# Kernel tuning notes

Measured on AMD Instinct MI355X. Metric: run time of the kernel, lower is better.

The kernel has to match this reference:

```python
import jax, jax.numpy as jnp
import numpy as np

N = 100000
E = 1600000
EPS = 1e-5


def _bn(h, g, b):
    # BatchNorm1d in training mode: batch stats over dim 0 (biased variance)
    mu = h.mean(0)
    var = ((h - mu) ** 2).mean(0)
    return g * (h - mu) * jax.lax.rsqrt(var + EPS) + b


def setup_inputs() -> dict:
    key = jax.random.key(0)

    def nrm(i, shape, scale=1.0):
        return jax.random.normal(jax.random.fold_in(key, i), shape, jnp.float32) * scale

    inp = {
        "x": nrm(0, (N, 1)),
        "edge_attr": nrm(1, (E, 2)),
        "edge_index": jax.random.randint(jax.random.fold_in(key, 2), (2, E), 0, N),
        "dir_edge_index": jax.random.randint(jax.random.fold_in(key, 3), (2, E), 0, N),
        "prop_edge_index": jax.random.randint(jax.random.fold_in(key, 4), (2, E), 0, N),
    }
    k = [10]

    def lin(name, fan_in, fan_out):
        inp[name] = nrm(k[0], (fan_in, fan_out), 1.0 / float(np.sqrt(fan_in)))
        k[0] += 1

    def bnp(prefix, c):
        inp[prefix + "_g"] = jnp.ones((c,), jnp.float32)
        inp[prefix + "_b"] = jnp.zeros((c,), jnp.float32)

    lin("c1_ws", 1, 2); lin("c1_wn", 1, 2); lin("c1_we", 2, 2); bnp("c1", 2)
    lin("d1_ws", 3, 4); lin("d1_wn", 3, 4); bnp("d1", 4)
    lin("c2_ws", 5, 6); lin("c2_wn", 5, 6); lin("c2_we", 2, 6); bnp("c2", 6)
    lin("d2_ws", 7, 8); lin("d2_wn", 7, 8); bnp("d2", 8)
    lin("c3_ws", 9, 10); lin("c3_wn", 9, 10); lin("c3_we", 2, 10); bnp("c3", 10)
    lin("d3_ws", 11, 12); lin("d3_wn", 11, 12); bnp("d3", 12)
    lin("pw1", 13, 8); inp["pb1"] = jnp.zeros((8,), jnp.float32); bnp("p1", 8)
    lin("pw2", 8, 4); inp["pb2"] = jnp.zeros((4,), jnp.float32); bnp("p2", 4)
    lin("pw3", 4, 1); inp["pb3"] = jnp.zeros((1,), jnp.float32)
    lin("ew1", 28, 14); inp["eb1"] = jnp.zeros((14,), jnp.float32); bnp("e1", 14)
    lin("ew2", 14, 1); inp["eb2"] = jnp.zeros((1,), jnp.float32)
    return inp


def reference(x, edge_attr, edge_index, dir_edge_index, prop_edge_index,
              c1_ws, c1_wn, c1_we, c1_g, c1_b,
              d1_ws, d1_wn, d1_g, d1_b,
              c2_ws, c2_wn, c2_we, c2_g, c2_b,
              d2_ws, d2_wn, d2_g, d2_b,
              c3_ws, c3_wn, c3_we, c3_g, c3_b,
              d3_ws, d3_wn, d3_g, d3_b,
              pw1, pb1, p1_g, p1_b, pw2, pb2, p2_g, p2_b, pw3, pb3,
              ew1, eb1, e1_g, e1_b, ew2, eb2):
    n = x.shape[0]
    src, dst = edge_index[0], edge_index[1]        # x_j = x[src], x_i = x[dst]
    psrc, pdst = prop_edge_index[0], prop_edge_index[1]

    def flexconv(h, ws, wn, we, g, b):
        m = jax.nn.relu(_bn(h[dst] @ ws + edge_attr @ we + h[src] @ wn, g, b))
        agg = jax.ops.segment_sum(m, dst, num_segments=n)
        return jnp.concatenate([h[:, :1], agg], axis=1)

    def edgeinter(h, ws, wn, g, b):
        m = jax.nn.relu(_bn(h[pdst] @ ws + h[psrc] @ wn, g, b))
        agg = jax.ops.segment_sum(m, pdst, num_segments=n)
        return jnp.concatenate([h[:, :1], agg], axis=1)

    out = flexconv(x, c1_ws, c1_wn, c1_we, c1_g, c1_b)      # [N,3]
    out = edgeinter(out, d1_ws, d1_wn, d1_g, d1_b)          # [N,5]
    out = flexconv(out, c2_ws, c2_wn, c2_we, c2_g, c2_b)    # [N,7]
    out = edgeinter(out, d2_ws, d2_wn, d2_g, d2_b)          # [N,9]
    out = flexconv(out, c3_ws, c3_wn, c3_we, c3_g, c3_b)    # [N,11]
    out = edgeinter(out, d3_ws, d3_wn, d3_g, d3_b)          # [N,13]

    h = _bn(jax.nn.relu(out @ pw1 + pb1), p1_g, p1_b)
    h = _bn(jax.nn.relu(h @ pw2 + pb2), p2_g, p2_b)
    power = jax.nn.sigmoid(1.5 * (h @ pw3 + pb3))           # [N,1]

    dsrc, ddst = dir_edge_index[0], dir_edge_index[1]
    f = jnp.concatenate([out[ddst], power[ddst], out[dsrc], power[dsrc]], axis=1)  # [E,28]
    e = _bn(jax.nn.relu(f @ ew1 + eb1), e1_g, e1_b)
    direction = jax.nn.sigmoid(1.5 * (e @ ew2 + eb2))       # [E,1]
    return power, direction
```

## Files before the change

### kernel.cpp

```cpp
#include <hip/hip_runtime.h>
#include <hip/hip_fp16.h>
#include <math.h>

static constexpr int BLK = 256;
static constexpr float BN_EPS = 1e-5f;

__device__ __forceinline__ float sigmoid15(float z) {
    return 1.0f / (1.0f + expf(-1.5f * z));
}

__device__ __forceinline__ unsigned pack_ea(float2 v) {
    unsigned hx = __half_as_ushort(__float2half_rn(v.x));
    unsigned hy = __half_as_ushort(__float2half_rn(v.y));
    return hx | (hy << 16);
}
__device__ __forceinline__ float2 unpack_ea(unsigned u) {
    return make_float2(__half2float(__ushort_as_half((unsigned short)(u & 0xffffu))),
                       __half2float(__ushort_as_half((unsigned short)(u >> 16))));
}

template<int C>
__device__ __forceinline__ void block_stats_reduce(float (&s)[C], float (&ss)[C],
                                                   double* __restrict__ stats)
{
    #pragma unroll
    for (int j = 0; j < C; ++j) {
        #pragma unroll
        for (int o = 32; o > 0; o >>= 1) {
            s[j]  += __shfl_down(s[j],  o, 64);
            ss[j] += __shfl_down(ss[j], o, 64);
        }
    }
    __shared__ float red[2][C][BLK / 64];
    const int wave = threadIdx.x >> 6, lane = threadIdx.x & 63;
    if (lane == 0) {
        #pragma unroll
        for (int j = 0; j < C; ++j) { red[0][j][wave] = s[j]; red[1][j][wave] = ss[j]; }
    }
    __syncthreads();
    if (threadIdx.x < C) {
        const int j = threadIdx.x;
        float a = 0.f, b = 0.f;
        #pragma unroll
        for (int w = 0; w < BLK / 64; ++w) { a += red[0][j][w]; b += red[1][j][w]; }
        atomicAdd(&stats[j],      (double)a);
        atomicAdd(&stats[16 + j], (double)b);
    }
}

template<int C>
__device__ __forceinline__ void bn_coefs(const double* __restrict__ stats,
                                         const float* __restrict__ g, const float* __restrict__ b,
                                         double invE, float (&sc)[C], float (&bb)[C])
{
    #pragma unroll
    for (int j = 0; j < C; ++j) {
        const double mu  = stats[j] * invE;
        const double var = stats[16 + j] * invE - mu * mu;
        const float inv = rsqrtf((float)(var + (double)BN_EPS));
        const float gg = g[j];
        sc[j] = gg * inv;
        bb[j] = b[j] - (float)mu * gg * inv;
    }
}


__global__ __launch_bounds__(BLK) void init_kernel(int* __restrict__ deg, double* __restrict__ stats,
                                                   int* __restrict__ rowstart, int n2, int total)
{
    const int i = blockIdx.x * blockDim.x + threadIdx.x;
    if (i < n2) deg[i] = 0;
    if (i < 288) stats[i] = 0.0;
    if (i == 0) rowstart[n2] = total;
}

__global__ __launch_bounds__(BLK) void hist_kernel(const int* __restrict__ edst,
                                                   const int* __restrict__ pdst,
                                                   int* __restrict__ deg, int N, int E)
{
    const int grp = blockIdx.x & 7;
    const int bg  = blockIdx.x >> 3;
    const int gstride = (gridDim.x >> 3) * blockDim.x;
    if (grp < 4) {
        const int lo = (int)((size_t)N * grp / 4), hi = (int)((size_t)N * (grp + 1) / 4);
        for (int e = bg * blockDim.x + threadIdx.x; e < E; e += gstride) {
            const int d = edst[e];
            if (d >= lo && d < hi) atomicAdd(&deg[d], 1);
        }
    } else {
        const int gg = grp - 4;
        const int lo = (int)((size_t)N * gg / 4), hi = (int)((size_t)N * (gg + 1) / 4);
        for (int e = bg * blockDim.x + threadIdx.x; e < E; e += gstride) {
            const int p = pdst[e];
            if (p >= lo && p < hi) atomicAdd(&deg[N + p], 1);
        }
    }
}

__global__ __launch_bounds__(256) void scan1_kernel(const int* __restrict__ deg,
                                                    int* __restrict__ rowstart,
                                                    int* __restrict__ partials, int n2)
{
    __shared__ int lds[256];
    const int tid = threadIdx.x;
    const int base = blockIdx.x * 1024 + tid * 4;
    int v[4]; int loc = 0;
    #pragma unroll
    for (int r = 0; r < 4; ++r) { v[r] = (base + r < n2) ? deg[base + r] : 0; loc += v[r]; }
    lds[tid] = loc; __syncthreads();
    #pragma unroll
    for (int off = 1; off < 256; off <<= 1) {
        int t = (tid >= off) ? lds[tid - off] : 0;
        __syncthreads();
        lds[tid] += t;
        __syncthreads();
    }
    int excl = lds[tid] - loc;
    int run = excl;
    #pragma unroll
    for (int r = 0; r < 4; ++r) {
        if (base + r < n2) rowstart[base + r] = run;
        run += v[r];
    }
    if (tid == 255) partials[blockIdx.x] = lds[255];
}

__global__ __launch_bounds__(256) void scan2_kernel(int* __restrict__ partials, int n)
{
    __shared__ int lds[256];
    const int tid = threadIdx.x;
    const int base = tid * 4;
    int v[4]; int loc = 0;
    #pragma unroll
    for (int r = 0; r < 4; ++r) { v[r] = (base + r < n) ? partials[base + r] : 0; loc += v[r]; }
    lds[tid] = loc; __syncthreads();
    #pragma unroll
    for (int off = 1; off < 256; off <<= 1) {
        int t = (tid >= off) ? lds[tid - off] : 0;
        __syncthreads();
        lds[tid] += t;
        __syncthreads();
    }
    int excl = lds[tid] - loc;
    int run = excl;
    #pragma unroll
    for (int r = 0; r < 4; ++r) {
        if (base + r < n) partials[base + r] = run;
        run += v[r];
    }
}

__global__ __launch_bounds__(BLK) void scan3_kernel(int* __restrict__ rowstart,
                                                    int* __restrict__ cursor,
                                                    const int* __restrict__ partials, int n2)
{
    const int i = blockIdx.x * blockDim.x + threadIdx.x;
    if (i >= n2) return;
    const int v = rowstart[i] + partials[i >> 10];
    rowstart[i] = v;
    cursor[i] = v;
}

__global__ __launch_bounds__(BLK) void fill_kernel(
    const int* __restrict__ esrc, const int* __restrict__ edst,
    const int* __restrict__ psrc, const int* __restrict__ pdst,
    const float* __restrict__ ea,
    int* __restrict__ cursor, uint2* __restrict__ csr_e,
    unsigned int* __restrict__ csr_psrc, int N, int E)
{
    const int grp = blockIdx.x & 7;
    const int bg  = blockIdx.x >> 3;
    const int gstride = (gridDim.x >> 3) * blockDim.x;
    if (grp < 4) {
        const int lo = (int)((size_t)N * grp / 4), hi = (int)((size_t)N * (grp + 1) / 4);
        for (int e = bg * blockDim.x + threadIdx.x; e < E; e += gstride) {
            const int d = edst[e];
            if (d >= lo && d < hi) {
                const float2 eav = ((const float2*)ea)[e];
                const int pos = atomicAdd(&cursor[d], 1);
                csr_e[pos] = make_uint2((unsigned)esrc[e], pack_ea(eav));
            }
        }
    } else {
        const int gg = grp - 4;
        const int lo = (int)((size_t)N * gg / 4), hi = (int)((size_t)N * (gg + 1) / 4);
        for (int e = bg * blockDim.x + threadIdx.x; e < E; e += gstride) {
            const int p = pdst[e];
            if (p >= lo && p < hi) {
                const int pos2 = atomicAdd(&cursor[N + p], 1);
                csr_psrc[pos2 - E] = (unsigned)psrc[e];
            }
        }
    }
}


template<int CIN, int COUT>
__global__ __launch_bounds__(BLK) void projQ_kernel(
    const float* __restrict__ x, const float* __restrict__ agg_in,
    const float* __restrict__ wn, float* __restrict__ Q, int n)
{
    constexpr int PAD = (COUT + 3) & ~3;
    __shared__ float swn[CIN * COUT];
    for (int i = threadIdx.x; i < CIN * COUT; i += blockDim.x) swn[i] = wn[i];
    __syncthreads();
    const int i = blockIdx.x * blockDim.x + threadIdx.x;
    if (i >= n) return;
    float h[CIN];
    h[0] = x[i];
    #pragma unroll
    for (int k = 1; k < CIN; ++k) h[k] = agg_in[(size_t)i * (CIN - 1) + (k - 1)];
    #pragma unroll
    for (int j = 0; j < COUT; ++j) {
        float q = 0.f;
        #pragma unroll
        for (int k = 0; k < CIN; ++k) q = fmaf(h[k], swn[k * COUT + j], q);
        Q[(size_t)i * PAD + j] = q;
    }
}

template<int CIN, int COUT, bool HASEA>
__global__ __launch_bounds__(BLK) void node_stats_kernel(
    const int* __restrict__ rowstart,
    const uint2* __restrict__ csr_e, const unsigned int* __restrict__ csr_psrc,
    const float* __restrict__ x, const float* __restrict__ agg_in,
    const float* __restrict__ ws, const float* __restrict__ Q,
    const float* __restrict__ we,
    double* __restrict__ stats, int N, int base, int koff)
{
    constexpr int PAD = (COUT + 3) & ~3;
    __shared__ float sws[CIN * COUT];
    for (int i = threadIdx.x; i < CIN * COUT; i += blockDim.x) sws[i] = ws[i];
    __syncthreads();
    float we0[COUT], we1[COUT];
    if constexpr (HASEA) {
        #pragma unroll
        for (int j = 0; j < COUT; ++j) { we0[j] = we[j]; we1[j] = we[COUT + j]; }
    }
    float s[COUT], ss[COUT];
    #pragma unroll
    for (int j = 0; j < COUT; ++j) { s[j] = 0.f; ss[j] = 0.f; }
    const int t = blockIdx.x * blockDim.x + threadIdx.x;
    const int i = t >> 2, quad = t & 3;
    if (i < N) {
        float h[CIN];
        h[0] = x[i];
        #pragma unroll
        for (int k = 1; k < CIN; ++k) h[k] = agg_in[(size_t)i * (CIN - 1) + (k - 1)];
        float pp[COUT];
        #pragma unroll
        for (int j = 0; j < COUT; ++j) {
            float p = 0.f;
            #pragma unroll
            for (int k = 0; k < CIN; ++k) p = fmaf(h[k], sws[k * COUT + j], p);
            pp[j] = p;
        }
        const int k0 = rowstart[base + i], k1 = rowstart[base + i + 1];
        for (int k = k0 + quad; k < k1; k += 4) {
            unsigned sn;
            float2 eav;
            if constexpr (HASEA) {
                const uint2 ce = csr_e[k];
                sn = ce.x; eav = unpack_ea(ce.y);
            } else {
                sn = csr_psrc[k - koff];
            }
            #pragma unroll
            for (int j = 0; j < COUT; ++j) {
                float m = pp[j] + Q[(size_t)sn * PAD + j];
                if constexpr (HASEA) m = fmaf(eav.x, we0[j], fmaf(eav.y, we1[j], m));
                s[j] += m; ss[j] = fmaf(m, m, ss[j]);
            }
        }
    }
    block_stats_reduce<COUT>(s, ss, stats);
}

template<int CIN, int COUT, bool HASEA, int CIN2, int COUT2>
__global__ __launch_bounds__(BLK) void node_agg_kernel(
    const int* __restrict__ rowstart,
    const uint2* __restrict__ csr_e, const unsigned int* __restrict__ csr_psrc,
    const float* __restrict__ x, const float* __restrict__ agg_in,
    const float* __restrict__ ws, const float* __restrict__ Q,
    const float* __restrict__ we,
    const float* __restrict__ g, const float* __restrict__ b,
    const double* __restrict__ stats,
    float* __restrict__ agg_out,
    const float* __restrict__ wn2, float* __restrict__ Qout,
    int N, int base, int koff, float invE)
{
    constexpr int PAD = (COUT + 3) & ~3;
    constexpr bool FUSEQ = (COUT2 > 0);
    constexpr int W2 = FUSEQ ? CIN2 * COUT2 : 1;
    __shared__ float sws[CIN * COUT];
    __shared__ float swn2[W2];
    for (int i = threadIdx.x; i < CIN * COUT; i += blockDim.x) sws[i] = ws[i];
    if constexpr (FUSEQ) {
        for (int i = threadIdx.x; i < W2; i += blockDim.x) swn2[i] = wn2[i];
    }
    __syncthreads();
    const int t = blockIdx.x * blockDim.x + threadIdx.x;
    const int i = t >> 2, quad = t & 3;
    if (i >= N) return;
    float we0[COUT], we1[COUT];
    if constexpr (HASEA) {
        #pragma unroll
        for (int j = 0; j < COUT; ++j) { we0[j] = we[j]; we1[j] = we[COUT + j]; }
    }
    float sc[COUT], bb[COUT];
    bn_coefs<COUT>(stats, g, b, (double)invE, sc, bb);
    float h[CIN];
    h[0] = x[i];
    #pragma unroll
    for (int k = 1; k < CIN; ++k) h[k] = agg_in[(size_t)i * (CIN - 1) + (k - 1)];
    float pp[COUT], acc[COUT];
    #pragma unroll
    for (int j = 0; j < COUT; ++j) {
        float p = 0.f;
        #pragma unroll
        for (int k = 0; k < CIN; ++k) p = fmaf(h[k], sws[k * COUT + j], p);
        pp[j] = p; acc[j] = 0.f;
    }
    const int k0 = rowstart[base + i], k1 = rowstart[base + i + 1];
    for (int k = k0 + quad; k < k1; k += 4) {
        unsigned sn;
        float2 eav;
        if constexpr (HASEA) {
            const uint2 ce = csr_e[k];
            sn = ce.x; eav = unpack_ea(ce.y);
        } else {
            sn = csr_psrc[k - koff];
        }
        #pragma unroll
        for (int j = 0; j < COUT; ++j) {
            float m = pp[j] + Q[(size_t)sn * PAD + j];
            if constexpr (HASEA) m = fmaf(eav.x, we0[j], fmaf(eav.y, we1[j], m));
            acc[j] += fmaxf(fmaf(sc[j], m, bb[j]), 0.f);
        }
    }
    #pragma unroll
    for (int j = 0; j < COUT; ++j) {
        acc[j] += __shfl_xor(acc[j], 1, 64);
        acc[j] += __shfl_xor(acc[j], 2, 64);
    }
    if (quad == 0) {
        #pragma unroll
        for (int j = 0; j < COUT; ++j) agg_out[(size_t)i * COUT + j] = acc[j];
        if constexpr (FUSEQ) {
            constexpr int PAD2 = (COUT2 + 3) & ~3;
            #pragma unroll
            for (int j2 = 0; j2 < COUT2; ++j2) {
                float q = h[0] * swn2[j2];
                #pragma unroll
                for (int k = 0; k < COUT; ++k)
                    q = fmaf(acc[k], swn2[(k + 1) * COUT2 + j2], q);
                Qout[(size_t)i * PAD2 + j2] = q;
            }
        }
    }
}


__global__ __launch_bounds__(BLK) void zero_stats_kernel(double* __restrict__ stats, int n)
{
    int i = blockIdx.x * blockDim.x + threadIdx.x;
    if (i < n) stats[i] = 0.0;
}

template<int CIN, int COUT>
__global__ __launch_bounds__(BLK) void projPQ_kernel(
    const float* __restrict__ x, const float* __restrict__ agg_in,
    const float* __restrict__ ws, const float* __restrict__ wn,
    float* __restrict__ P, float* __restrict__ Q, float* __restrict__ agg_out, int n)
{
    __shared__ float sws[CIN * COUT], swn[CIN * COUT];
    for (int i = threadIdx.x; i < CIN * COUT; i += blockDim.x) { sws[i] = ws[i]; swn[i] = wn[i]; }
    __syncthreads();
    const int i = blockIdx.x * blockDim.x + threadIdx.x;
    if (i >= n) return;
    float h[CIN];
    h[0] = x[i];
    #pragma unroll
    for (int k = 1; k < CIN; ++k) h[k] = agg_in[(size_t)i * (CIN - 1) + (k - 1)];
    #pragma unroll
    for (int j = 0; j < COUT; ++j) {
        float p = 0.f, q = 0.f;
        #pragma unroll
        for (int k = 0; k < CIN; ++k) {
            p = fmaf(h[k], sws[k * COUT + j], p);
            q = fmaf(h[k], swn[k * COUT + j], q);
        }
        P[(size_t)i * COUT + j] = p;
        Q[(size_t)i * COUT + j] = q;
        agg_out[(size_t)i * COUT + j] = 0.f;
    }
}

template<int COUT, bool HASEA>
__global__ __launch_bounds__(BLK) void edge_stats_kernel(
    const int* __restrict__ esrc, const int* __restrict__ edst,
    const float* __restrict__ P,  const float* __restrict__ Q,
    const float* __restrict__ ea, const float* __restrict__ we,
    double* __restrict__ stats, int E)
{
    float we0[COUT], we1[COUT];
    if constexpr (HASEA) {
        #pragma unroll
        for (int j = 0; j < COUT; ++j) { we0[j] = we[j]; we1[j] = we[COUT + j]; }
    }
    float s[COUT], ss[COUT];
    #pragma unroll
    for (int j = 0; j < COUT; ++j) { s[j] = 0.f; ss[j] = 0.f; }
    const int stride = gridDim.x * blockDim.x;
    for (int e = blockIdx.x * blockDim.x + threadIdx.x; e < E; e += stride) {
        const int d = edst[e], sn = esrc[e];
        float2 eav = make_float2(0.f, 0.f);
        if constexpr (HASEA) eav = ((const float2* __restrict__)ea)[e];
        #pragma unroll
        for (int j = 0; j < COUT; ++j) {
            float m = P[(size_t)d * COUT + j] + Q[(size_t)sn * COUT + j];
            if constexpr (HASEA) m += eav.x * we0[j] + eav.y * we1[j];
            s[j] += m; ss[j] = fmaf(m, m, ss[j]);
        }
    }
    block_stats_reduce<COUT>(s, ss, stats);
}

template<int COUT, bool HASEA>
__global__ __launch_bounds__(BLK) void edge_scatter_kernel(
    const int* __restrict__ esrc, const int* __restrict__ edst,
    const float* __restrict__ P,  const float* __restrict__ Q,
    const float* __restrict__ ea, const float* __restrict__ we,
    const float* __restrict__ g,  const float* __restrict__ b,
    const double* __restrict__ stats,
    float* __restrict__ agg_out, int E)
{
    float we0[COUT], we1[COUT], sc[COUT], bb[COUT];
    #pragma unroll
    for (int j = 0; j < COUT; ++j) {
        if constexpr (HASEA) { we0[j] = we[j]; we1[j] = we[COUT + j]; }
    }
    bn_coefs<COUT>(stats, g, b, 1.0 / (double)E, sc, bb);
    const int stride = gridDim.x * blockDim.x;
    for (int e = blockIdx.x * blockDim.x + threadIdx.x; e < E; e += stride) {
        const int d = edst[e], sn = esrc[e];
        float2 eav = make_float2(0.f, 0.f);
        if constexpr (HASEA) eav = ((const float2* __restrict__)ea)[e];
        #pragma unroll
        for (int j = 0; j < COUT; ++j) {
            float m = P[(size_t)d * COUT + j] + Q[(size_t)sn * COUT + j];
            if constexpr (HASEA) m += eav.x * we0[j] + eav.y * we1[j];
            const float y = fmaxf(fmaf(sc[j], m, bb[j]), 0.f);
            if (y > 0.f) unsafeAtomicAdd(&agg_out[(size_t)d * COUT + j], y);
        }
    }
}


__global__ __launch_bounds__(BLK) void mlp1_kernel(
    const float* __restrict__ x, const float* __restrict__ agg6,
    const float* __restrict__ pw1, const float* __restrict__ pb1,
    float* __restrict__ t1, double* __restrict__ stats, int n)
{
    __shared__ float w[13 * 8];
    __shared__ float bsh[8];
    for (int i = threadIdx.x; i < 13 * 8; i += blockDim.x) w[i] = pw1[i];
    if (threadIdx.x < 8) bsh[threadIdx.x] = pb1[threadIdx.x];
    __syncthreads();
    const int i = blockIdx.x * blockDim.x + threadIdx.x;
    float s[8], ss[8];
    #pragma unroll
    for (int j = 0; j < 8; ++j) { s[j] = 0.f; ss[j] = 0.f; }
    if (i < n) {
        float h[13];
        h[0] = x[i];
        #pragma unroll
        for (int k = 0; k < 12; ++k) h[k + 1] = agg6[(size_t)i * 12 + k];
        #pragma unroll
        for (int j = 0; j < 8; ++j) {
            float t = bsh[j];
            #pragma unroll
            for (int k = 0; k < 13; ++k) t = fmaf(h[k], w[k * 8 + j], t);
            t = fmaxf(t, 0.f);
            t1[(size_t)i * 8 + j] = t;
            s[j] = t; ss[j] = t * t;
        }
    }
    block_stats_reduce<8>(s, ss, stats);
}

__global__ __launch_bounds__(BLK) void mlp2_kernel(
    const float* __restrict__ t1,
    const float* __restrict__ p1g, const float* __restrict__ p1b,
    const float* __restrict__ pw2, const float* __restrict__ pb2,
    const double* __restrict__ stats1,
    float* __restrict__ t2, double* __restrict__ stats2, int n)
{
    float sc[8], bb[8];
    bn_coefs<8>(stats1, p1g, p1b, 1.0 / (double)n, sc, bb);
    const int i = blockIdx.x * blockDim.x + threadIdx.x;
    float s[4], ss[4];
    #pragma unroll
    for (int j = 0; j < 4; ++j) { s[j] = 0.f; ss[j] = 0.f; }
    if (i < n) {
        float u[8];
        #pragma unroll
        for (int j = 0; j < 8; ++j) u[j] = fmaf(sc[j], t1[(size_t)i * 8 + j], bb[j]);
        #pragma unroll
        for (int j2 = 0; j2 < 4; ++j2) {
            float t = pb2[j2];
            #pragma unroll
            for (int j = 0; j < 8; ++j) t = fmaf(u[j], pw2[j * 4 + j2], t);
            t = fmaxf(t, 0.f);
            t2[(size_t)i * 4 + j2] = t;
            s[j2] = t; ss[j2] = t * t;
        }
    }
    block_stats_reduce<4>(s, ss, stats2);
}

__global__ __launch_bounds__(BLK) void mlp3_kernel(
    const float* __restrict__ t2,
    const float* __restrict__ p2g, const float* __restrict__ p2b,
    const float* __restrict__ pw3, const float* __restrict__ pb3,
    const float* __restrict__ x, const float* __restrict__ agg6,
    const float* __restrict__ ew1, const float* __restrict__ eb1,
    const double* __restrict__ stats2,
    float* __restrict__ power_out, float* __restrict__ A, float* __restrict__ B,
    int n, int astride)
{
    __shared__ float w1[28 * 14];
    for (int i = threadIdx.x; i < 28 * 14; i += blockDim.x) w1[i] = ew1[i];
    __syncthreads();
    float sc[4], bb[4];
    bn_coefs<4>(stats2, p2g, p2b, 1.0 / (double)n, sc, bb);
    const int i = blockIdx.x * blockDim.x + threadIdx.x;
    if (i >= n) return;
    float z = pb3[0];
    #pragma unroll
    for (int j = 0; j < 4; ++j) z = fmaf(fmaf(sc[j], t2[(size_t)i * 4 + j], bb[j]), pw3[j], z);
    const float pw = sigmoid15(z);
    power_out[i] = pw;
    float h[14];
    h[0] = x[i];
    #pragma unroll
    for (int k = 0; k < 12; ++k) h[k + 1] = agg6[(size_t)i * 12 + k];
    h[13] = pw;
    #pragma unroll
    for (int c = 0; c < 14; ++c) {
        float a = eb1[c], b2 = 0.f;
        #pragma unroll
        for (int k = 0; k < 14; ++k) {
            a  = fmaf(h[k], w1[k * 14 + c], a);
            b2 = fmaf(h[k], w1[(14 + k) * 14 + c], b2);
        }
        A[(size_t)i * astride + c] = a;
        B[(size_t)i * astride + c] = b2;
    }
}

__global__ __launch_bounds__(BLK) void ehead_stats_kernel(
    const int* __restrict__ dsrc, const int* __restrict__ ddst,
    const float* __restrict__ A, const float* __restrict__ B,
    double* __restrict__ stats, int E, int astride)
{
    float s[14], ss[14];
    #pragma unroll
    for (int j = 0; j < 14; ++j) { s[j] = 0.f; ss[j] = 0.f; }
    const int stride = gridDim.x * blockDim.x;
    for (int e = blockIdx.x * blockDim.x + threadIdx.x; e < E; e += stride) {
        const int dd = ddst[e], ds = dsrc[e];
        #pragma unroll
        for (int c = 0; c < 14; ++c) {
            const float r = fmaxf(A[(size_t)dd * astride + c] + B[(size_t)ds * astride + c], 0.f);
            s[c] += r; ss[c] = fmaf(r, r, ss[c]);
        }
    }
    block_stats_reduce<14>(s, ss, stats);
}

__global__ __launch_bounds__(BLK) void ehead_final_kernel(
    const int* __restrict__ dsrc, const int* __restrict__ ddst,
    const float* __restrict__ A, const float* __restrict__ B,
    const float* __restrict__ e1g, const float* __restrict__ e1b,
    const float* __restrict__ ew2, const float* __restrict__ eb2,
    const double* __restrict__ stats, float* __restrict__ dir_out, int E, int astride)
{
    float sc[14];
    float off = eb2[0];
    const double invE = 1.0 / (double)E;
    #pragma unroll
    for (int c = 0; c < 14; ++c) {
        const double mu  = stats[c] * invE;
        const double var = stats[16 + c] * invE - mu * mu;
        const float inv = rsqrtf((float)(var + (double)BN_EPS));
        const float gi = e1g[c] * inv;
        sc[c] = gi * ew2[c];
        off += (e1b[c] - (float)mu * gi) * ew2[c];
    }
    const int stride = gridDim.x * blockDim.x;
    for (int e = blockIdx.x * blockDim.x + threadIdx.x; e < E; e += stride) {
        const int dd = ddst[e], ds = dsrc[e];
        float z = off;
        #pragma unroll
        for (int c = 0; c < 14; ++c) {
            const float r = fmaxf(A[(size_t)dd * astride + c] + B[(size_t)ds * astride + c], 0.f);
            z = fmaf(r, sc[c], z);
        }
        dir_out[e] = sigmoid15(z);
    }
}


extern "C" void kernel_launch(void* const* d_in, const int* in_sizes, int n_in,
                              void* d_out, int out_size, void* d_ws, size_t ws_size,
                              hipStream_t stream)
{
    const float* x    = (const float*)d_in[0];
    const float* ea   = (const float*)d_in[1];
    const int*   eidx = (const int*)d_in[2];
    const int*   didx = (const int*)d_in[3];
    const int*   pidx = (const int*)d_in[4];
    const float *c1_ws=(const float*)d_in[5],  *c1_wn=(const float*)d_in[6],  *c1_we=(const float*)d_in[7],  *c1_g=(const float*)d_in[8],  *c1_b=(const float*)d_in[9];
    const float *d1_ws=(const float*)d_in[10], *d1_wn=(const float*)d_in[11], *d1_g=(const float*)d_in[12], *d1_b=(const float*)d_in[13];
    const float *c2_ws=(const float*)d_in[14], *c2_wn=(const float*)d_in[15], *c2_we=(const float*)d_in[16], *c2_g=(const float*)d_in[17], *c2_b=(const float*)d_in[18];
    const float *d2_ws=(const float*)d_in[19], *d2_wn=(const float*)d_in[20], *d2_g=(const float*)d_in[21], *d2_b=(const float*)d_in[22];
    const float *c3_ws=(const float*)d_in[23], *c3_wn=(const float*)d_in[24], *c3_we=(const float*)d_in[25], *c3_g=(const float*)d_in[26], *c3_b=(const float*)d_in[27];
    const float *d3_ws=(const float*)d_in[28], *d3_wn=(const float*)d_in[29], *d3_g=(const float*)d_in[30], *d3_b=(const float*)d_in[31];
    const float *pw1=(const float*)d_in[32], *pb1=(const float*)d_in[33], *p1_g=(const float*)d_in[34], *p1_b=(const float*)d_in[35];
    const float *pw2=(const float*)d_in[36], *pb2=(const float*)d_in[37], *p2_g=(const float*)d_in[38], *p2_b=(const float*)d_in[39];
    const float *pw3=(const float*)d_in[40], *pb3=(const float*)d_in[41];
    const float *ew1=(const float*)d_in[42], *eb1=(const float*)d_in[43], *e1_g=(const float*)d_in[44], *e1_b=(const float*)d_in[45];
    const float *ew2=(const float*)d_in[46], *eb2=(const float*)d_in[47];

    const int N = in_sizes[0];
    const int E = in_sizes[2] / 2;
    const int n2 = 2 * N;
    const int *esrc = eidx,     *edst = eidx + E;
    const int *dsrc = didx,     *ddst = didx + E;
    const int *psrc = pidx,     *pdst = pidx + E;

    float* power_out = (float*)d_out;
    float* dir_out   = power_out + N;

    const int gN  = (N + BLK - 1) / BLK;
    const int g2  = (n2 + BLK - 1) / BLK;
    const int g4  = ((size_t)4 * N + BLK - 1) / BLK;
    const int gE  = 1024;
    const int gEf = (E + BLK - 1) / BLK;
    const int gX  = 8 * 160;
    const float invE = 1.0f / (float)E;

    const size_t abFloats = (size_t)32 * N;
    const size_t csreBytes = ((size_t)8 * E > 4 * abFloats) ? (size_t)8 * E : 4 * abFloats;
    const size_t need_csr = 4096
        + sizeof(float) * ((size_t)N * 12
                         + (size_t)N * 12
                         + (size_t)N * 12
                         + (size_t)N * 12)
        + csreBytes
        + sizeof(unsigned int) * (size_t)E
        + sizeof(int) * ((size_t)n2 + 2)
        + sizeof(int) * (size_t)n2
        + sizeof(int) * 1024;

    double* stats = (double*)d_ws;

    if (ws_size >= need_csr) {
        float* fws  = (float*)((char*)d_ws + 4096);
        float* Qa   = fws;                fws += (size_t)N * 12;
        float* Qb   = fws;                fws += (size_t)N * 12;
        float* aggA = fws;                fws += (size_t)N * 12;
        float* aggB = fws;                fws += (size_t)N * 12;
        uint2* csr_e = (uint2*)fws;
        unsigned int* csr_psrc = (unsigned int*)((char*)csr_e + csreBytes);
        int* rowstart = (int*)(csr_psrc + E);
        int* cursor   = rowstart + (n2 + 2);
        int* deg      = cursor;
        int* partials = cursor + n2;
        float* t1   = aggA;
        float* t2   = aggA + (size_t)N * 8;
        float* Abuf = (float*)csr_e;
        float* Bbuf = Abuf + (size_t)N * 16;

        const int nparts = (n2 + 1023) / 1024;

        init_kernel<<<g2, BLK, 0, stream>>>(deg, stats, rowstart, n2, 2 * E);
        hist_kernel<<<gX, BLK, 0, stream>>>(edst, pdst, deg, N, E);
        scan1_kernel<<<nparts, 256, 0, stream>>>(deg, rowstart, partials, n2);
        scan2_kernel<<<1, 256, 0, stream>>>(partials, nparts);
        scan3_kernel<<<g2, BLK, 0, stream>>>(rowstart, cursor, partials, n2);
        fill_kernel<<<gX, BLK, 0, stream>>>(esrc, edst, psrc, pdst, ea, cursor, csr_e, csr_psrc, N, E);

        projQ_kernel<1, 2><<<gN, BLK, 0, stream>>>(x, nullptr, c1_wn, Qa, N);
        node_stats_kernel<1, 2, true><<<g4, BLK, 0, stream>>>(rowstart, csr_e, csr_psrc, x, nullptr, c1_ws, Qa, c1_we, stats + 0, N, 0, 0);
        node_agg_kernel<1, 2, true, 3, 4><<<g4, BLK, 0, stream>>>(rowstart, csr_e, csr_psrc, x, nullptr, c1_ws, Qa, c1_we, c1_g, c1_b, stats + 0, aggA, d1_wn, Qb, N, 0, 0, invE);
        node_stats_kernel<3, 4, false><<<g4, BLK, 0, stream>>>(rowstart, csr_e, csr_psrc, x, aggA, d1_ws, Qb, nullptr, stats + 32, N, N, E);
        node_agg_kernel<3, 4, false, 5, 6><<<g4, BLK, 0, stream>>>(rowstart, csr_e, csr_psrc, x, aggA, d1_ws, Qb, nullptr, d1_g, d1_b, stats + 32, aggB, c2_wn, Qa, N, N, E, invE);
        node_stats_kernel<5, 6, true><<<g4, BLK, 0, stream>>>(rowstart, csr_e, csr_psrc, x, aggB, c2_ws, Qa, c2_we, stats + 64, N, 0, 0);
        node_agg_kernel<5, 6, true, 7, 8><<<g4, BLK, 0, stream>>>(rowstart, csr_e, csr_psrc, x, aggB, c2_ws, Qa, c2_we, c2_g, c2_b, stats + 64, aggA, d2_wn, Qb, N, 0, 0, invE);
        node_stats_kernel<7, 8, false><<<g4, BLK, 0, stream>>>(rowstart, csr_e, csr_psrc, x, aggA, d2_ws, Qb, nullptr, stats + 96, N, N, E);
        node_agg_kernel<7, 8, false, 9, 10><<<g4, BLK, 0, stream>>>(rowstart, csr_e, csr_psrc, x, aggA, d2_ws, Qb, nullptr, d2_g, d2_b, stats + 96, aggB, c3_wn, Qa, N, N, E, invE);
        node_stats_kernel<9, 10, true><<<g4, BLK, 0, stream>>>(rowstart, csr_e, csr_psrc, x, aggB, c3_ws, Qa, c3_we, stats + 128, N, 0, 0);
        node_agg_kernel<9, 10, true, 11, 12><<<g4, BLK, 0, stream>>>(rowstart, csr_e, csr_psrc, x, aggB, c3_ws, Qa, c3_we, c3_g, c3_b, stats + 128, aggA, d3_wn, Qb, N, 0, 0, invE);
        node_stats_kernel<11, 12, false><<<g4, BLK, 0, stream>>>(rowstart, csr_e, csr_psrc, x, aggA, d3_ws, Qb, nullptr, stats + 160, N, N, E);
        node_agg_kernel<11, 12, false, 0, 0><<<g4, BLK, 0, stream>>>(rowstart, csr_e, csr_psrc, x, aggA, d3_ws, Qb, nullptr, d3_g, d3_b, stats + 160, aggB, nullptr, nullptr, N, N, E, invE);

        mlp1_kernel<<<gN, BLK, 0, stream>>>(x, aggB, pw1, pb1, t1, stats + 192, N);
        mlp2_kernel<<<gN, BLK, 0, stream>>>(t1, p1_g, p1_b, pw2, pb2, stats + 192, t2, stats + 224, N);
        mlp3_kernel<<<gN, BLK, 0, stream>>>(t2, p2_g, p2_b, pw3, pb3, x, aggB, ew1, eb1, stats + 224,
                                            power_out, Abuf, Bbuf, N, 16);
        ehead_stats_kernel<<<gE, BLK, 0, stream>>>(dsrc, ddst, Abuf, Bbuf, stats + 256, E, 16);
        ehead_final_kernel<<<gEf, BLK, 0, stream>>>(dsrc, ddst, Abuf, Bbuf, e1_g, e1_b, ew2, eb2,
                                                    stats + 256, dir_out, E, 16);
    } else {
        float* fws  = (float*)((char*)d_ws + 4096);
        float* P    = fws;                fws += (size_t)N * 14;
        float* Q    = fws;                fws += (size_t)N * 14;
        float* aggA = fws;                fws += (size_t)N * 12;
        float* aggB = fws;                fws += (size_t)N * 12;
        float* t1   = aggA;
        float* t2   = aggA + (size_t)N * 8;
        float* Abuf = P;
        float* Bbuf = Q;

        zero_stats_kernel<<<2, BLK, 0, stream>>>(stats, 288);

        projPQ_kernel<1, 2><<<gN, BLK, 0, stream>>>(x, nullptr, c1_ws, c1_wn, P, Q, aggA, N);
        edge_stats_kernel<2, true><<<gE, BLK, 0, stream>>>(esrc, edst, P, Q, ea, c1_we, stats + 0, E);
        edge_scatter_kernel<2, true><<<gE, BLK, 0, stream>>>(esrc, edst, P, Q, ea, c1_we, c1_g, c1_b, stats + 0, aggA, E);

        projPQ_kernel<3, 4><<<gN, BLK, 0, stream>>>(x, aggA, d1_ws, d1_wn, P, Q, aggB, N);
        edge_stats_kernel<4, false><<<gE, BLK, 0, stream>>>(psrc, pdst, P, Q, nullptr, nullptr, stats + 32, E);
        edge_scatter_kernel<4, false><<<gE, BLK, 0, stream>>>(psrc, pdst, P, Q, nullptr, nullptr, d1_g, d1_b, stats + 32, aggB, E);

        projPQ_kernel<5, 6><<<gN, BLK, 0, stream>>>(x, aggB, c2_ws, c2_wn, P, Q, aggA, N);
        edge_stats_kernel<6, true><<<gE, BLK, 0, stream>>>(esrc, edst, P, Q, ea, c2_we, stats + 64, E);
        edge_scatter_kernel<6, true><<<gE, BLK, 0, stream>>>(esrc, edst, P, Q, ea, c2_we, c2_g, c2_b, stats + 64, aggA, E);

        projPQ_kernel<7, 8><<<gN, BLK, 0, stream>>>(x, aggA, d2_ws, d2_wn, P, Q, aggB, N);
        edge_stats_kernel<8, false><<<gE, BLK, 0, stream>>>(psrc, pdst, P, Q, nullptr, nullptr, stats + 96, E);
        edge_scatter_kernel<8, false><<<gE, BLK, 0, stream>>>(psrc, pdst, P, Q, nullptr, nullptr, d2_g, d2_b, stats + 96, aggB, E);

        projPQ_kernel<9, 10><<<gN, BLK, 0, stream>>>(x, aggB, c3_ws, c3_wn, P, Q, aggA, N);
        edge_stats_kernel<10, true><<<gE, BLK, 0, stream>>>(esrc, edst, P, Q, ea, c3_we, stats + 128, E);
        edge_scatter_kernel<10, true><<<gE, BLK, 0, stream>>>(esrc, edst, P, Q, ea, c3_we, c3_g, c3_b, stats + 128, aggA, E);

        projPQ_kernel<11, 12><<<gN, BLK, 0, stream>>>(x, aggA, d3_ws, d3_wn, P, Q, aggB, N);
        edge_stats_kernel<12, false><<<gE, BLK, 0, stream>>>(psrc, pdst, P, Q, nullptr, nullptr, stats + 160, E);
        edge_scatter_kernel<12, false><<<gE, BLK, 0, stream>>>(psrc, pdst, P, Q, nullptr, nullptr, d3_g, d3_b, stats + 160, aggB, E);

        mlp1_kernel<<<gN, BLK, 0, stream>>>(x, aggB, pw1, pb1, t1, stats + 192, N);
        mlp2_kernel<<<gN, BLK, 0, stream>>>(t1, p1_g, p1_b, pw2, pb2, stats + 192, t2, stats + 224, N);
        mlp3_kernel<<<gN, BLK, 0, stream>>>(t2, p2_g, p2_b, pw3, pb3, x, aggB, ew1, eb1, stats + 224,
                                            power_out, Abuf, Bbuf, N, 14);
        ehead_stats_kernel<<<gE, BLK, 0, stream>>>(dsrc, ddst, Abuf, Bbuf, stats + 256, E, 14);
        ehead_final_kernel<<<gE, BLK, 0, stream>>>(dsrc, ddst, Abuf, Bbuf, e1_g, e1_b, ew2, eb2,
                                                   stats + 256, dir_out, E, 14);
    }
}
```

Measured before the change: 952.1 us.

## Store gathered node tables in fp16 padded rows and stream edge indices nontemporally

The per-node Q projection tables and the edge-head A/B tables are now stored as fp16 rows padded to 8 or 16 halves and read with 16-byte vector loads. The aim is to cut the bytes moved by the random per-edge gathers. Edge index and attribute reads in the histogram, fill and edge-head kernels use nontemporal loads to reduce cache pollution. The trade-off is fp16 rounding of intermediate projections that feed BatchNorm statistics, which can cost accuracy.

```diff
diff --git a/kernel.cpp b/kernel.cpp
--- a/kernel.cpp
+++ b/kernel.cpp
@@ -17,6 +17,39 @@
 __device__ __forceinline__ float2 unpack_ea(unsigned u) {
     return make_float2(__half2float(__ushort_as_half((unsigned short)(u & 0xffffu))),
                        __half2float(__ushort_as_half((unsigned short)(u >> 16))));
+}
+
+__host__ __device__ constexpr int padh(int c) { return (c <= 8) ? 8 : 16; }
+
+template<int C>
+__device__ __forceinline__ void load_hrow(const __half* __restrict__ T, size_t row, float (&q)[C])
+{
+    constexpr int PADH = padh(C);
+    const uint4* p = (const uint4*)(T + row * PADH);
+    unsigned w[PADH / 2];
+    uint4 r0 = p[0];
+    w[0] = r0.x; w[1] = r0.y; w[2] = r0.z; w[3] = r0.w;
+    if constexpr (C > 8) { uint4 r1 = p[1]; w[4] = r1.x; w[5] = r1.y; w[6] = r1.z; w[7] = r1.w; }
+    #pragma unroll
+    for (int j = 0; j < C; ++j) {
+        unsigned h = (w[j >> 1] >> ((j & 1) * 16)) & 0xffffu;
+        q[j] = __half2float(__ushort_as_half((unsigned short)h));
+    }
+}
+
+template<int C>
+__device__ __forceinline__ void store_hrow(__half* __restrict__ T, size_t row, const float (&q)[C])
+{
+    constexpr int PADH = padh(C);
+    unsigned w[PADH / 2] = {0};
+    #pragma unroll
+    for (int j = 0; j < C; ++j) {
+        unsigned h = __half_as_ushort(__float2half_rn(q[j]));
+        w[j >> 1] |= h << ((j & 1) * 16);
+    }
+    uint4* p = (uint4*)(T + row * PADH);
+    p[0] = make_uint4(w[0], w[1], w[2], w[3]);
+    if constexpr (C > 8) p[1] = make_uint4(w[4], w[5], w[6], w[7]);
 }
 
 template<int C>
@@ -84,14 +117,14 @@
     if (grp < 4) {
         const int lo = (int)((size_t)N * grp / 4), hi = (int)((size_t)N * (grp + 1) / 4);
         for (int e = bg * blockDim.x + threadIdx.x; e < E; e += gstride) {
-            const int d = edst[e];
+            const int d = __builtin_nontemporal_load(&edst[e]);
             if (d >= lo && d < hi) atomicAdd(&deg[d], 1);
         }
     } else {
         const int gg = grp - 4;
         const int lo = (int)((size_t)N * gg / 4), hi = (int)((size_t)N * (gg + 1) / 4);
         for (int e = bg * blockDim.x + threadIdx.x; e < E; e += gstride) {
-            const int p = pdst[e];
+            const int p = __builtin_nontemporal_load(&pdst[e]);
             if (p >= lo && p < hi) atomicAdd(&deg[N + p], 1);
         }
     }
@@ -174,21 +207,24 @@
     if (grp < 4) {
         const int lo = (int)((size_t)N * grp / 4), hi = (int)((size_t)N * (grp + 1) / 4);
         for (int e = bg * blockDim.x + threadIdx.x; e < E; e += gstride) {
-            const int d = edst[e];
+            const int d = __builtin_nontemporal_load(&edst[e]);
             if (d >= lo && d < hi) {
-                const float2 eav = ((const float2*)ea)[e];
+                const double eabits = __builtin_nontemporal_load((const double*)ea + e);
+                float2 eav; __builtin_memcpy(&eav, &eabits, 8);
+                const int sn = __builtin_nontemporal_load(&esrc[e]);
                 const int pos = atomicAdd(&cursor[d], 1);
-                csr_e[pos] = make_uint2((unsigned)esrc[e], pack_ea(eav));
+                csr_e[pos] = make_uint2((unsigned)sn, pack_ea(eav));
             }
         }
     } else {
         const int gg = grp - 4;
         const int lo = (int)((size_t)N * gg / 4), hi = (int)((size_t)N * (gg + 1) / 4);
         for (int e = bg * blockDim.x + threadIdx.x; e < E; e += gstride) {
-            const int p = pdst[e];
+            const int p = __builtin_nontemporal_load(&pdst[e]);
             if (p >= lo && p < hi) {
+                const int sn = __builtin_nontemporal_load(&psrc[e]);
                 const int pos2 = atomicAdd(&cursor[N + p], 1);
-                csr_psrc[pos2 - E] = (unsigned)psrc[e];
+                csr_psrc[pos2 - E] = (unsigned)sn;
             }
         }
     }
@@ -198,9 +234,8 @@
 template<int CIN, int COUT>
 __global__ __launch_bounds__(BLK) void projQ_kernel(
     const float* __restrict__ x, const float* __restrict__ agg_in,
-    const float* __restrict__ wn, float* __restrict__ Q, int n)
-{
-    constexpr int PAD = (COUT + 3) & ~3;
+    const float* __restrict__ wn, __half* __restrict__ Q, int n)
+{
     __shared__ float swn[CIN * COUT];
     for (int i = threadIdx.x; i < CIN * COUT; i += blockDim.x) swn[i] = wn[i];
     __syncthreads();
@@ -210,13 +245,15 @@
     h[0] = x[i];
     #pragma unroll
     for (int k = 1; k < CIN; ++k) h[k] = agg_in[(size_t)i * (CIN - 1) + (k - 1)];
+    float q[COUT];
     #pragma unroll
     for (int j = 0; j < COUT; ++j) {
-        float q = 0.f;
-        #pragma unroll
-        for (int k = 0; k < CIN; ++k) q = fmaf(h[k], swn[k * COUT + j], q);
-        Q[(size_t)i * PAD + j] = q;
-    }
+        float qq = 0.f;
+        #pragma unroll
+        for (int k = 0; k < CIN; ++k) qq = fmaf(h[k], swn[k * COUT + j], qq);
+        q[j] = qq;
+    }
+    store_hrow<COUT>(Q, (size_t)i, q);
 }
 
 template<int CIN, int COUT, bool HASEA>
@@ -224,11 +261,10 @@
     const int* __restrict__ rowstart,
     const uint2* __restrict__ csr_e, const unsigned int* __restrict__ csr_psrc,
     const float* __restrict__ x, const float* __restrict__ agg_in,
-    const float* __restrict__ ws, const float* __restrict__ Q,
+    const float* __restrict__ ws, const __half* __restrict__ Q,
     const float* __restrict__ we,
     double* __restrict__ stats, int N, int base, int koff)
 {
-    constexpr int PAD = (COUT + 3) & ~3;
     __shared__ float sws[CIN * COUT];
     for (int i = threadIdx.x; i < CIN * COUT; i += blockDim.x) sws[i] = ws[i];
     __syncthreads();
@@ -265,9 +301,11 @@
             } else {
                 sn = csr_psrc[k - koff];
             }
+            float qr[COUT];
+            load_hrow<COUT>(Q, (size_t)sn, qr);
             #pragma unroll
             for (int j = 0; j < COUT; ++j) {
-                float m = pp[j] + Q[(size_t)sn * PAD + j];
+                float m = pp[j] + qr[j];
                 if constexpr (HASEA) m = fmaf(eav.x, we0[j], fmaf(eav.y, we1[j], m));
                 s[j] += m; ss[j] = fmaf(m, m, ss[j]);
             }
@@ -281,15 +319,14 @@
     const int* __restrict__ rowstart,
     const uint2* __restrict__ csr_e, const unsigned int* __restrict__ csr_psrc,
     const float* __restrict__ x, const float* __restrict__ agg_in,
-    const float* __restrict__ ws, const float* __restrict__ Q,
+    const float* __restrict__ ws, const __half* __restrict__ Q,
     const float* __restrict__ we,
     const float* __restrict__ g, const float* __restrict__ b,
     const double* __restrict__ stats,
     float* __restrict__ agg_out,
-    const float* __restrict__ wn2, float* __restrict__ Qout,
+    const float* __restrict__ wn2, __half* __restrict__ Qout,
     int N, int base, int koff, float invE)
 {
-    constexpr int PAD = (COUT + 3) & ~3;
     constexpr bool FUSEQ = (COUT2 > 0);
     constexpr int W2 = FUSEQ ? CIN2 * COUT2 : 1;
     __shared__ float sws[CIN * COUT];
@@ -331,9 +368,11 @@
         } else {
             sn = csr_psrc[k - koff];
         }
+        float qr[COUT];
+        load_hrow<COUT>(Q, (size_t)sn, qr);
         #pragma unroll
         for (int j = 0; j < COUT; ++j) {
-            float m = pp[j] + Q[(size_t)sn * PAD + j];
+            float m = pp[j] + qr[j];
             if constexpr (HASEA) m = fmaf(eav.x, we0[j], fmaf(eav.y, we1[j], m));
             acc[j] += fmaxf(fmaf(sc[j], m, bb[j]), 0.f);
         }
@@ -347,15 +386,16 @@
         #pragma unroll
         for (int j = 0; j < COUT; ++j) agg_out[(size_t)i * COUT + j] = acc[j];
         if constexpr (FUSEQ) {
-            constexpr int PAD2 = (COUT2 + 3) & ~3;
+            float qrow[COUT2 > 0 ? COUT2 : 1];
             #pragma unroll
             for (int j2 = 0; j2 < COUT2; ++j2) {
                 float q = h[0] * swn2[j2];
                 #pragma unroll
                 for (int k = 0; k < COUT; ++k)
                     q = fmaf(acc[k], swn2[(k + 1) * COUT2 + j2], q);
-                Qout[(size_t)i * PAD2 + j2] = q;
+                qrow[j2] = q;
             }
+            store_hrow<COUT2>(Qout, (size_t)i, qrow);
         }
     }
 }
@@ -526,8 +566,7 @@
     const float* __restrict__ x, const float* __restrict__ agg6,
     const float* __restrict__ ew1, const float* __restrict__ eb1,
     const double* __restrict__ stats2,
-    float* __restrict__ power_out, float* __restrict__ A, float* __restrict__ B,
-    int n, int astride)
+    float* __restrict__ power_out, __half* __restrict__ A, __half* __restrict__ B, int n)
 {
     __shared__ float w1[28 * 14];
     for (int i = threadIdx.x; i < 28 * 14; i += blockDim.x) w1[i] = ew1[i];
@@ -546,6 +585,7 @@
     #pragma unroll
     for (int k = 0; k < 12; ++k) h[k + 1] = agg6[(size_t)i * 12 + k];
     h[13] = pw;
+    float arow[14], brow[14];
     #pragma unroll
     for (int c = 0; c < 14; ++c) {
         float a = eb1[c], b2 = 0.f;
@@ -554,25 +594,30 @@
             a  = fmaf(h[k], w1[k * 14 + c], a);
             b2 = fmaf(h[k], w1[(14 + k) * 14 + c], b2);
         }
-        A[(size_t)i * astride + c] = a;
-        B[(size_t)i * astride + c] = b2;
-    }
+        arow[c] = a; brow[c] = b2;
+    }
+    store_hrow<14>(A, (size_t)i, arow);
+    store_hrow<14>(B, (size_t)i, brow);
 }
 
 __global__ __launch_bounds__(BLK) void ehead_stats_kernel(
     const int* __restrict__ dsrc, const int* __restrict__ ddst,
-    const float* __restrict__ A, const float* __restrict__ B,
-    double* __restrict__ stats, int E, int astride)
+    const __half* __restrict__ A, const __half* __restrict__ B,
+    double* __restrict__ stats, int E)
 {
     float s[14], ss[14];
     #pragma unroll
     for (int j = 0; j < 14; ++j) { s[j] = 0.f; ss[j] = 0.f; }
     const int stride = gridDim.x * blockDim.x;
     for (int e = blockIdx.x * blockDim.x + threadIdx.x; e < E; e += stride) {
-        const int dd = ddst[e], ds = dsrc[e];
+        const int dd = __builtin_nontemporal_load(&ddst[e]);
+        const int ds = __builtin_nontemporal_load(&dsrc[e]);
+        float ar[14], br[14];
+        load_hrow<14>(A, (size_t)dd, ar);
+        load_hrow<14>(B, (size_t)ds, br);
         #pragma unroll
         for (int c = 0; c < 14; ++c) {
-            const float r = fmaxf(A[(size_t)dd * astride + c] + B[(size_t)ds * astride + c], 0.f);
+            const float r = fmaxf(ar[c] + br[c], 0.f);
             s[c] += r; ss[c] = fmaf(r, r, ss[c]);
         }
     }
@@ -581,10 +626,10 @@
 
 __global__ __launch_bounds__(BLK) void ehead_final_kernel(
     const int* __restrict__ dsrc, const int* __restrict__ ddst,
-    const float* __restrict__ A, const float* __restrict__ B,
+    const __half* __restrict__ A, const __half* __restrict__ B,
     const float* __restrict__ e1g, const float* __restrict__ e1b,
     const float* __restrict__ ew2, const float* __restrict__ eb2,
-    const double* __restrict__ stats, float* __restrict__ dir_out, int E, int astride)
+    const double* __restrict__ stats, float* __restrict__ dir_out, int E)
 {
     float sc[14];
     float off = eb2[0];
@@ -600,11 +645,15 @@
     }
     const int stride = gridDim.x * blockDim.x;
     for (int e = blockIdx.x * blockDim.x + threadIdx.x; e < E; e += stride) {
-        const int dd = ddst[e], ds = dsrc[e];
+        const int dd = __builtin_nontemporal_load(&ddst[e]);
+        const int ds = __builtin_nontemporal_load(&dsrc[e]);
+        float ar[14], br[14];
+        load_hrow<14>(A, (size_t)dd, ar);
+        load_hrow<14>(B, (size_t)ds, br);
         float z = off;
         #pragma unroll
         for (int c = 0; c < 14; ++c) {
-            const float r = fmaxf(A[(size_t)dd * astride + c] + B[(size_t)ds * astride + c], 0.f);
+            const float r = fmaxf(ar[c] + br[c], 0.f);
             z = fmaf(r, sc[c], z);
         }
         dir_out[e] = sigmoid15(z);
@@ -651,12 +700,12 @@
     const int gX  = 8 * 160;
     const float invE = 1.0f / (float)E;
 
-    const size_t abFloats = (size_t)32 * N;
-    const size_t csreBytes = ((size_t)8 * E > 4 * abFloats) ? (size_t)8 * E : 4 * abFloats;
+    const size_t abBytes = (size_t)2 * N * 16 * sizeof(__half);
+    const size_t csreBytes0 = (size_t)8 * E;
+    const size_t csreBytes = (csreBytes0 > abBytes) ? csreBytes0 : abBytes;
     const size_t need_csr = 4096
+        + sizeof(__half) * (size_t)N * 16 * 2
         + sizeof(float) * ((size_t)N * 12
-                         + (size_t)N * 12
-                         + (size_t)N * 12
                          + (size_t)N * 12)
         + csreBytes
         + sizeof(unsigned int) * (size_t)E
@@ -667,21 +716,21 @@
     double* stats = (double*)d_ws;
 
     if (ws_size >= need_csr) {
-        float* fws  = (float*)((char*)d_ws + 4096);
-        float* Qa   = fws;                fws += (size_t)N * 12;
-        float* Qb   = fws;                fws += (size_t)N * 12;
-        float* aggA = fws;                fws += (size_t)N * 12;
-        float* aggB = fws;                fws += (size_t)N * 12;
-        uint2* csr_e = (uint2*)fws;
-        unsigned int* csr_psrc = (unsigned int*)((char*)csr_e + csreBytes);
-        int* rowstart = (int*)(csr_psrc + E);
-        int* cursor   = rowstart + (n2 + 2);
+        char* p = (char*)d_ws + 4096;
+        __half* Qa = (__half*)p;          p += sizeof(__half) * (size_t)N * 16;
+        __half* Qb = (__half*)p;          p += sizeof(__half) * (size_t)N * 16;
+        float* aggA = (float*)p;          p += sizeof(float) * (size_t)N * 12;
+        float* aggB = (float*)p;          p += sizeof(float) * (size_t)N * 12;
+        uint2* csr_e = (uint2*)p;         p += csreBytes;
+        unsigned int* csr_psrc = (unsigned int*)p;  p += sizeof(unsigned int) * (size_t)E;
+        int* rowstart = (int*)p;          p += sizeof(int) * ((size_t)n2 + 2);
+        int* cursor   = (int*)p;
         int* deg      = cursor;
         int* partials = cursor + n2;
         float* t1   = aggA;
         float* t2   = aggA + (size_t)N * 8;
-        float* Abuf = (float*)csr_e;
-        float* Bbuf = Abuf + (size_t)N * 16;
+        __half* Abuf = (__half*)csr_e;
+        __half* Bbuf = Abuf + (size_t)N * 16;
 
         const int nparts = (n2 + 1023) / 1024;
 
@@ -709,10 +758,10 @@
         mlp1_kernel<<<gN, BLK, 0, stream>>>(x, aggB, pw1, pb1, t1, stats + 192, N);
         mlp2_kernel<<<gN, BLK, 0, stream>>>(t1, p1_g, p1_b, pw2, pb2, stats + 192, t2, stats + 224, N);
         mlp3_kernel<<<gN, BLK, 0, stream>>>(t2, p2_g, p2_b, pw3, pb3, x, aggB, ew1, eb1, stats + 224,
-                                            power_out, Abuf, Bbuf, N, 16);
-        ehead_stats_kernel<<<gE, BLK, 0, stream>>>(dsrc, ddst, Abuf, Bbuf, stats + 256, E, 16);
+                                            power_out, Abuf, Bbuf, N);
+        ehead_stats_kernel<<<gE, BLK, 0, stream>>>(dsrc, ddst, Abuf, Bbuf, stats + 256, E);
         ehead_final_kernel<<<gEf, BLK, 0, stream>>>(dsrc, ddst, Abuf, Bbuf, e1_g, e1_b, ew2, eb2,
-                                                    stats + 256, dir_out, E, 16);
+                                                    stats + 256, dir_out, E);
     } else {
         float* fws  = (float*)((char*)d_ws + 4096);
         float* P    = fws;                fws += (size_t)N * 14;
@@ -721,8 +770,8 @@
         float* aggB = fws;                fws += (size_t)N * 12;
         float* t1   = aggA;
         float* t2   = aggA + (size_t)N * 8;
-        float* Abuf = P;
-        float* Bbuf = Q;
+        __half* Abuf = (__half*)P;
+        __half* Bbuf = (__half*)Q;
 
         zero_stats_kernel<<<2, BLK, 0, stream>>>(stats, 288);
 
@@ -753,9 +802,9 @@
         mlp1_kernel<<<gN, BLK, 0, stream>>>(x, aggB, pw1, pb1, t1, stats + 192, N);
         mlp2_kernel<<<gN, BLK, 0, stream>>>(t1, p1_g, p1_b, pw2, pb2, stats + 192, t2, stats + 224, N);
         mlp3_kernel<<<gN, BLK, 0, stream>>>(t2, p2_g, p2_b, pw3, pb3, x, aggB, ew1, eb1, stats + 224,
-                                            power_out, Abuf, Bbuf, N, 14);
-        ehead_stats_kernel<<<gE, BLK, 0, stream>>>(dsrc, ddst, Abuf, Bbuf, stats + 256, E, 14);
+                                            power_out, Abuf, Bbuf, N);
+        ehead_stats_kernel<<<gE, BLK, 0, stream>>>(dsrc, ddst, Abuf, Bbuf, stats + 256, E);
         ehead_final_kernel<<<gE, BLK, 0, stream>>>(dsrc, ddst, Abuf, Bbuf, e1_g, e1_b, ew2, eb2,
-                                                   stats + 256, dir_out, E, 14);
-    }
-}
+                                                   stats + 256, dir_out, E);
+    }
+}
```

Measured after the change: 892.2 us. -6.3%, faster.
